# Kernel optimization log

Measured on AMD Instinct MI355X. Metric: run time of the kernel, lower is better.

## Reference

```python
import jax, jax.numpy as jnp
import numpy as np

B, T, D, H, O, L = 64, 1024, 64, 512, 1, 1


def setup_inputs() -> dict:
    key = jax.random.key(0)
    k = jax.random.split(key, 6)
    s = 1.0 / np.sqrt(H)  # PyTorch GRU init scale U(-1/sqrt(H), 1/sqrt(H))
    x = jax.random.normal(k[0], (B, T, D), dtype=jnp.float32)
    h = jnp.zeros((L, B, H), dtype=jnp.float32)
    w_ih = jax.random.uniform(k[1], (3 * H, D), jnp.float32, -s, s)
    w_hh = jax.random.uniform(k[2], (3 * H, H), jnp.float32, -s, s)
    fc_w = jax.random.uniform(k[3], (O, H), jnp.float32, -s, s)
    fc_b = jax.random.uniform(k[4], (O,), jnp.float32, -s, s)
    return {"x": x, "h": h, "w_ih": w_ih, "w_hh": w_hh, "fc_w": fc_w, "fc_b": fc_b}


def _gru_layer(x, h0, w_ih, w_hh):
    # x: [B,T,D], h0: [B,H]. bias=False GRU, PyTorch gate order r,z,n.
    Hd = w_hh.shape[1]
    gi_all = jnp.einsum('btd,gd->tbg', x, w_ih)  # [T,B,3H] input projections, one big GEMM

    def step(h, gi):
        gh = h @ w_hh.T  # [B,3H]
        r = jax.nn.sigmoid(gi[:, :Hd] + gh[:, :Hd])
        z = jax.nn.sigmoid(gi[:, Hd:2 * Hd] + gh[:, Hd:2 * Hd])
        n = jnp.tanh(gi[:, 2 * Hd:] + r * gh[:, 2 * Hd:])
        h_new = (1.0 - z) * n + z * h
        return h_new, h_new

    h_last, hs = jax.lax.scan(step, h0, gi_all)  # hs: [T,B,H]
    return jnp.swapaxes(hs, 0, 1), h_last  # [B,T,H], [B,H]


def reference(x, h, w_ih, w_hh, fc_w, fc_b):
    out_seq, h_last = _gru_layer(x, h[0], w_ih, w_hh)
    out = jax.nn.relu(out_seq) @ fc_w.T + fc_b  # [B,T,O]
    return out, h_last[None]  # h: [n_layers=1, B, H]
```

## Files before the change

kernel.cpp:

```cpp
#include <hip/hip_runtime.h>

typedef short bf16x8 __attribute__((ext_vector_type(8)));
typedef float f32x4  __attribute__((ext_vector_type(4)));
typedef unsigned int u32;
typedef unsigned long long u64;

constexpr int BB = 64;
constexpr int TT = 1024;
constexpr int DD = 64;
constexpr int HH = 512;
constexpr int NGRP = 8;
constexpr int WPG  = 16;
constexpr int MB   = 8;
constexpr int UPW  = 32;
constexpr int BLOCK = 384;

constexpr size_t SLAB_U64  = (size_t)MB * 256;
constexpr size_t BOARD_U64 = 2 * NGRP * SLAB_U64;
constexpr size_t BOARD_B   = BOARD_U64 * 8;

__device__ __forceinline__ short f2bf(float f) {
    unsigned u = __builtin_bit_cast(unsigned, f);
    u = (u + 0x7FFFu + ((u >> 16) & 1u)) >> 16;
    return (short)u;
}
__device__ __forceinline__ float bf2f(short s) {
    unsigned u = ((unsigned)(unsigned short)s) << 16;
    return __builtin_bit_cast(float, u);
}

constexpr int LROW = 80;
constexpr int LKK  = 656;

__global__ __launch_bounds__(BLOCK, 2)
void gru_persistent(const float* __restrict__ x,
                    const float* __restrict__ h0,
                    const float* __restrict__ w_ih,
                    const float* __restrict__ w_hh,
                    const float* __restrict__ fc_w,
                    const float* __restrict__ fc_b,
                    float* __restrict__ out,
                    u64* __restrict__ board)
{
    const int wg   = blockIdx.x;
    const int gb   = wg & 7;
    const int wid  = wg >> 3;
    const int tid  = threadIdx.x;
    const int wave = tid >> 6;
    const int lane = tid & 63;
    const int l15  = lane & 15;
    const int lhi  = lane >> 4;
    const int u0   = wid * UPW;

    const int cloc = wave * 16 + l15;
    const int grow = (cloc >> 5) * HH + u0 + (cloc & 31);

    __shared__ char  lds_board[16 * LKK];
    __shared__ float lds_gi[8][100];
    __shared__ float lds_gh[8][100];
    __shared__ float fcw_lds[HH];

    bf16x8 whh_hi[16], whh_lo[16];
#pragma unroll
    for (int kk = 0; kk < 16; ++kk) {
        const float* src = w_hh + (size_t)grow * HH + kk * 32 + lhi * 8;
        bf16x8 hi, lo;
#pragma unroll
        for (int i = 0; i < 8; ++i) {
            float w = src[i];
            short h16 = f2bf(w);
            hi[i] = h16; lo[i] = f2bf(w - bf2f(h16));
        }
        whh_hi[kk] = hi; whh_lo[kk] = lo;
    }
    bf16x8 wih_hi[2], wih_lo[2];
#pragma unroll
    for (int kk = 0; kk < 2; ++kk) {
        const float* src = w_ih + (size_t)grow * DD + kk * 32 + lhi * 8;
        bf16x8 hi, lo;
#pragma unroll
        for (int i = 0; i < 8; ++i) {
            float w = src[i];
            short h16 = f2bf(w);
            hi[i] = h16; lo[i] = f2bf(w - bf2f(h16));
        }
        wih_hi[kk] = hi; wih_lo[kk] = lo;
    }

    for (int i = tid; i < HH; i += BLOCK) fcw_lds[i] = fc_w[i];
    const float fcb = fc_b[0];

    float hreg0 = 0.f, hreg1 = 0.f;
    if (tid < 128) {
        int row = tid >> 4, lp = tid & 15;
        hreg0 = h0[(size_t)(gb * MB + row) * HH + (u0 + 2 * lp)];
        hreg1 = h0[(size_t)(gb * MB + row) * HH + (u0 + 2 * lp + 1)];
        u32 wa = (1u << 16) | (u32)(unsigned short)f2bf(hreg0);
        u32 wb = (1u << 16) | (u32)(unsigned short)f2bf(hreg1);
        u64* bw = board + (size_t)(0 * NGRP + gb) * SLAB_U64 + row * 256 + (wid * 16 + lp);
        __hip_atomic_store(bw, (u64)wa | ((u64)wb << 32),
                           __ATOMIC_RELAXED, __HIP_MEMORY_SCOPE_AGENT);
    }
    __syncthreads();

    const float* xrow = x + ((size_t)(gb * MB + (l15 & 7)) * TT) * DD + lhi * 8;

    for (int t = 0; t <= TT; ++t) {
        const int rbuf = t & 1, wbuf = rbuf ^ 1;

        u64 v[8];
        const u64* sp = board + (size_t)(rbuf * NGRP + gb) * SLAB_U64 + tid;
        if (tid < 256) {
#pragma unroll
            for (int i = 0; i < 8; ++i)
                v[i] = __hip_atomic_load(sp + (size_t)i * 256,
                                         __ATOMIC_RELAXED, __HIP_MEMORY_SCOPE_AGENT);
        }

        f32x4 acc_gi = {0.f, 0.f, 0.f, 0.f};
        if (t < TT) {
            f32x4 gi_hi = {0.f,0.f,0.f,0.f}, gi_lo = {0.f,0.f,0.f,0.f};
#pragma unroll
            for (int kk = 0; kk < 2; ++kk) {
                const float* xs = xrow + (size_t)t * DD + kk * 32;
                const float4 v0 = *(const float4*)(xs);
                const float4 v1 = *(const float4*)(xs + 4);
                bf16x8 a;
                a[0] = f2bf(v0.x); a[1] = f2bf(v0.y); a[2] = f2bf(v0.z); a[3] = f2bf(v0.w);
                a[4] = f2bf(v1.x); a[5] = f2bf(v1.y); a[6] = f2bf(v1.z); a[7] = f2bf(v1.w);
                gi_hi = __builtin_amdgcn_mfma_f32_16x16x32_bf16(a, wih_hi[kk], gi_hi, 0, 0, 0);
                gi_lo = __builtin_amdgcn_mfma_f32_16x16x32_bf16(a, wih_lo[kk], gi_lo, 0, 0, 0);
            }
            acc_gi = gi_hi + gi_lo;
        }

        if (tid < 256) {
            const u32 expTag = (u32)(t + 1) << 16;
            while (true) {
                u32 bad = 0;
#pragma unroll
                for (int i = 0; i < 8; ++i) {
                    u32 lo = (u32)v[i], hi = (u32)(v[i] >> 32);
                    bad |= ((lo ^ expTag) | (hi ^ expTag)) & 0xFFFF0000u;
                }
                if (!__any(bad != 0)) break;
#pragma unroll
                for (int i = 0; i < 8; ++i)
                    v[i] = __hip_atomic_load(sp + (size_t)i * 256,
                                             __ATOMIC_RELAXED, __HIP_MEMORY_SCOPE_AGENT);
            }
            char* lb = lds_board + (tid >> 4) * LKK + (tid & 15) * 4;
#pragma unroll
            for (int i = 0; i < 8; ++i) {
                u32 d = __builtin_amdgcn_perm((u32)(v[i] >> 32), (u32)v[i], 0x05040100u);
                *(u32*)(lb + i * LROW) = d;
            }
        }
        __syncthreads();

        if (wave == 0 && wid < MB && t >= 1) {
            const char* lb = lds_board + (lane >> 2) * LKK + wid * LROW + (lane & 3) * 16;
            bf16x8 hv = *(const bf16x8*)lb;
            float s = 0.f;
#pragma unroll
            for (int i = 0; i < 8; ++i)
                s += fmaxf(bf2f(hv[i]), 0.f) * fcw_lds[lane * 8 + i];
#pragma unroll
            for (int off = 1; off < 64; off <<= 1) s += __shfl_xor(s, off, 64);
            if (lane == 0)
                out[(size_t)(gb * MB + wid) * TT + (t - 1)] = s + fcb;
        }
        if (t == TT) break;

        f32x4 gh_hi = {0.f,0.f,0.f,0.f}, gh_lo = {0.f,0.f,0.f,0.f};
        {
            const char* la = lds_board + (l15 & 7) * LROW + lhi * 16;
#pragma unroll
            for (int kk = 0; kk < 16; ++kk) {
                bf16x8 a = *(const bf16x8*)(la + kk * LKK);
                gh_hi = __builtin_amdgcn_mfma_f32_16x16x32_bf16(a, whh_hi[kk], gh_hi, 0, 0, 0);
                gh_lo = __builtin_amdgcn_mfma_f32_16x16x32_bf16(a, whh_lo[kk], gh_lo, 0, 0, 0);
            }
        }
        f32x4 acc_gh = gh_hi + gh_lo;

        if (lhi < 2) {
#pragma unroll
            for (int j = 0; j < 4; ++j) {
                int row = lhi * 4 + j;
                lds_gi[row][cloc] = acc_gi[j];
                lds_gh[row][cloc] = acc_gh[j];
            }
        }
        __syncthreads();

        if (tid < 128) {
            const u32 tagNew = (u32)(t + 2) << 16;
            int row = tid >> 4, lp = tid & 15;
            int uu0 = 2 * lp, uu1 = uu0 + 1;
            float hn01[2];
            float hp[2] = {hreg0, hreg1};
#pragma unroll
            for (int q = 0; q < 2; ++q) {
                int uu = uu0 + q;
                float gr  = lds_gi[row][uu]      + lds_gh[row][uu];
                float gz  = lds_gi[row][32 + uu] + lds_gh[row][32 + uu];
                float gin = lds_gi[row][64 + uu];
                float ghn = lds_gh[row][64 + uu];
                float r = 1.f / (1.f + __expf(-gr));
                float z = 1.f / (1.f + __expf(-gz));
                float vv = gin + r * ghn;
                vv = fminf(15.f, fmaxf(-15.f, vv));
                float e2 = __expf(-2.f * vv);
                float n = (1.f - e2) / (1.f + e2);
                hn01[q] = (1.f - z) * n + z * hp[q];
            }
            hreg0 = hn01[0]; hreg1 = hn01[1];
            u32 wa = tagNew | (u32)(unsigned short)f2bf(hn01[0]);
            u32 wb = tagNew | (u32)(unsigned short)f2bf(hn01[1]);
            u64* bw = board + (size_t)(wbuf * NGRP + gb) * SLAB_U64
                    + row * 256 + (wid * 16 + lp);
            __hip_atomic_store(bw, (u64)wa | ((u64)wb << 32),
                               __ATOMIC_RELAXED, __HIP_MEMORY_SCOPE_AGENT);
            if (t == TT - 1) {
                out[(size_t)BB * TT + (size_t)(gb * MB + row) * HH + (u0 + uu0)] = hn01[0];
                out[(size_t)BB * TT + (size_t)(gb * MB + row) * HH + (u0 + uu1)] = hn01[1];
            }
        }
    }
}

extern "C" void kernel_launch(void* const* d_in, const int* in_sizes, int n_in,
                              void* d_out, int out_size, void* d_ws, size_t ws_size,
                              hipStream_t stream)
{
    const float* x    = (const float*)d_in[0];
    const float* h0   = (const float*)d_in[1];
    const float* w_ih = (const float*)d_in[2];
    const float* w_hh = (const float*)d_in[3];
    const float* fc_w = (const float*)d_in[4];
    const float* fc_b = (const float*)d_in[5];
    float* out = (float*)d_out;
    u64* board = (u64*)d_ws;

    hipMemsetAsync(d_ws, 0, BOARD_B, stream);

    void* args[] = { (void*)&x, (void*)&h0, (void*)&w_ih, (void*)&w_hh,
                     (void*)&fc_w, (void*)&fc_b, (void*)&out, (void*)&board };
    hipError_t err = hipLaunchCooperativeKernel((void*)gru_persistent,
                                                dim3(NGRP * WPG), dim3(BLOCK),
                                                args, 0, stream);
    if (err != hipSuccess) {
        (void)hipGetLastError();
        gru_persistent<<<dim3(NGRP * WPG), dim3(BLOCK), 0, stream>>>(
            x, h0, w_ih, w_hh, fc_w, fc_b, out, board);
    }
}
```

Measured before the change: 2.855 ms.

## Split each batch group into two interleaved sub-batches to overlap recurrence latency

Each workgroup now processes its 8 batch rows as two independent sub-batches of 4, alternating between them within each timestep. While one sub-batch's hidden state is being computed and published to the global board, the other sub-batch's board slab is prefetched and waited on, which is meant to hide cross-workgroup synchronisation latency. The board gains a sub-batch dimension and per-element stores become 32-bit. In exchange there are twice as many barriers and MFMA passes per step, each with half the useful rows, and the MFMA row utilisation drops.

Result: slower. 3.903 ms (+36.7%).

```diff
diff --git a/kernel.cpp b/kernel.cpp
--- a/kernel.cpp
+++ b/kernel.cpp
@@ -11,13 +11,18 @@
 constexpr int HH = 512;
 constexpr int NGRP = 8;
 constexpr int WPG  = 16;
-constexpr int MB   = 8;
+constexpr int NSB  = 2;
+constexpr int MB   = 4;
 constexpr int UPW  = 32;
 constexpr int BLOCK = 384;
 
 constexpr size_t SLAB_U64  = (size_t)MB * 256;
-constexpr size_t BOARD_U64 = 2 * NGRP * SLAB_U64;
+constexpr size_t BOARD_U64 = 2 * NSB * NGRP * SLAB_U64;
 constexpr size_t BOARD_B   = BOARD_U64 * 8;
+
+__device__ __forceinline__ size_t slab(int buf, int s, int g) {
+    return ((size_t)(buf * NSB + s) * NGRP + g) * SLAB_U64;
+}
 
 __device__ __forceinline__ short f2bf(float f) {
     unsigned u = __builtin_bit_cast(unsigned, f);
@@ -30,7 +35,7 @@
 }
 
 constexpr int LROW = 80;
-constexpr int LKK  = 656;
+constexpr int LKK  = 336;
 
 __global__ __launch_bounds__(BLOCK, 2)
 void gru_persistent(const float* __restrict__ x,
@@ -56,8 +61,8 @@
     const int grow = (cloc >> 5) * HH + u0 + (cloc & 31);
 
     __shared__ char  lds_board[16 * LKK];
-    __shared__ float lds_gi[8][100];
-    __shared__ float lds_gh[8][100];
+    __shared__ float lds_gi[4][100];
+    __shared__ float lds_gh[4][100];
     __shared__ float fcw_lds[HH];
 
     bf16x8 whh_hi[16], whh_lo[16];
@@ -90,119 +95,135 @@
     for (int i = tid; i < HH; i += BLOCK) fcw_lds[i] = fc_w[i];
     const float fcb = fc_b[0];
 
-    float hreg0 = 0.f, hreg1 = 0.f;
+    float hreg[NSB] = {0.f, 0.f};
     if (tid < 128) {
-        int row = tid >> 4, lp = tid & 15;
-        hreg0 = h0[(size_t)(gb * MB + row) * HH + (u0 + 2 * lp)];
-        hreg1 = h0[(size_t)(gb * MB + row) * HH + (u0 + 2 * lp + 1)];
-        u32 wa = (1u << 16) | (u32)(unsigned short)f2bf(hreg0);
-        u32 wb = (1u << 16) | (u32)(unsigned short)f2bf(hreg1);
-        u64* bw = board + (size_t)(0 * NGRP + gb) * SLAB_U64 + row * 256 + (wid * 16 + lp);
-        __hip_atomic_store(bw, (u64)wa | ((u64)wb << 32),
-                           __ATOMIC_RELAXED, __HIP_MEMORY_SCOPE_AGENT);
+        int row = tid >> 5, uu = tid & 31;
+#pragma unroll
+        for (int s = 0; s < NSB; ++s) {
+            float hv = h0[(size_t)(gb * 8 + s * MB + row) * HH + u0 + uu];
+            hreg[s] = hv;
+            u32 w = (1u << 16) | (u32)(unsigned short)f2bf(hv);
+            u32* bw = (u32*)(board + slab(0, s, gb)) + row * 512 + wid * 32 + uu;
+            __hip_atomic_store(bw, w, __ATOMIC_RELAXED, __HIP_MEMORY_SCOPE_AGENT);
+        }
     }
     __syncthreads();
 
-    const float* xrow = x + ((size_t)(gb * MB + (l15 & 7)) * TT) * DD + lhi * 8;
+    const float* xrow[NSB];
+#pragma unroll
+    for (int s = 0; s < NSB; ++s)
+        xrow[s] = x + ((size_t)(gb * 8 + s * MB + (l15 & 3)) * TT) * DD + lhi * 8;
+
+    u64 v[4];
+    const u64* sp = board + slab(0, 0, gb) + tid;
+    if (tid < 256) {
+#pragma unroll
+        for (int i = 0; i < 4; ++i)
+            v[i] = __hip_atomic_load(sp + (size_t)i * 256,
+                                     __ATOMIC_RELAXED, __HIP_MEMORY_SCOPE_AGENT);
+    }
 
     for (int t = 0; t <= TT; ++t) {
-        const int rbuf = t & 1, wbuf = rbuf ^ 1;
-
-        u64 v[8];
-        const u64* sp = board + (size_t)(rbuf * NGRP + gb) * SLAB_U64 + tid;
-        if (tid < 256) {
-#pragma unroll
-            for (int i = 0; i < 8; ++i)
-                v[i] = __hip_atomic_load(sp + (size_t)i * 256,
-                                         __ATOMIC_RELAXED, __HIP_MEMORY_SCOPE_AGENT);
-        }
-
-        f32x4 acc_gi = {0.f, 0.f, 0.f, 0.f};
-        if (t < TT) {
-            f32x4 gi_hi = {0.f,0.f,0.f,0.f}, gi_lo = {0.f,0.f,0.f,0.f};
-#pragma unroll
-            for (int kk = 0; kk < 2; ++kk) {
-                const float* xs = xrow + (size_t)t * DD + kk * 32;
-                const float4 v0 = *(const float4*)(xs);
-                const float4 v1 = *(const float4*)(xs + 4);
-                bf16x8 a;
-                a[0] = f2bf(v0.x); a[1] = f2bf(v0.y); a[2] = f2bf(v0.z); a[3] = f2bf(v0.w);
-                a[4] = f2bf(v1.x); a[5] = f2bf(v1.y); a[6] = f2bf(v1.z); a[7] = f2bf(v1.w);
-                gi_hi = __builtin_amdgcn_mfma_f32_16x16x32_bf16(a, wih_hi[kk], gi_hi, 0, 0, 0);
-                gi_lo = __builtin_amdgcn_mfma_f32_16x16x32_bf16(a, wih_lo[kk], gi_lo, 0, 0, 0);
-            }
-            acc_gi = gi_hi + gi_lo;
-        }
-
-        if (tid < 256) {
-            const u32 expTag = (u32)(t + 1) << 16;
-            while (true) {
-                u32 bad = 0;
-#pragma unroll
-                for (int i = 0; i < 8; ++i) {
-                    u32 lo = (u32)v[i], hi = (u32)(v[i] >> 32);
-                    bad |= ((lo ^ expTag) | (hi ^ expTag)) & 0xFFFF0000u;
-                }
-                if (!__any(bad != 0)) break;
-#pragma unroll
-                for (int i = 0; i < 8; ++i)
-                    v[i] = __hip_atomic_load(sp + (size_t)i * 256,
-                                             __ATOMIC_RELAXED, __HIP_MEMORY_SCOPE_AGENT);
-            }
-            char* lb = lds_board + (tid >> 4) * LKK + (tid & 15) * 4;
-#pragma unroll
-            for (int i = 0; i < 8; ++i) {
-                u32 d = __builtin_amdgcn_perm((u32)(v[i] >> 32), (u32)v[i], 0x05040100u);
-                *(u32*)(lb + i * LROW) = d;
-            }
-        }
-        __syncthreads();
-
-        if (wave == 0 && wid < MB && t >= 1) {
-            const char* lb = lds_board + (lane >> 2) * LKK + wid * LROW + (lane & 3) * 16;
-            bf16x8 hv = *(const bf16x8*)lb;
-            float s = 0.f;
-#pragma unroll
-            for (int i = 0; i < 8; ++i)
-                s += fmaxf(bf2f(hv[i]), 0.f) * fcw_lds[lane * 8 + i];
-#pragma unroll
-            for (int off = 1; off < 64; off <<= 1) s += __shfl_xor(s, off, 64);
-            if (lane == 0)
-                out[(size_t)(gb * MB + wid) * TT + (t - 1)] = s + fcb;
-        }
-        if (t == TT) break;
-
-        f32x4 gh_hi = {0.f,0.f,0.f,0.f}, gh_lo = {0.f,0.f,0.f,0.f};
-        {
-            const char* la = lds_board + (l15 & 7) * LROW + lhi * 16;
-#pragma unroll
-            for (int kk = 0; kk < 16; ++kk) {
-                bf16x8 a = *(const bf16x8*)(la + kk * LKK);
-                gh_hi = __builtin_amdgcn_mfma_f32_16x16x32_bf16(a, whh_hi[kk], gh_hi, 0, 0, 0);
-                gh_lo = __builtin_amdgcn_mfma_f32_16x16x32_bf16(a, whh_lo[kk], gh_lo, 0, 0, 0);
-            }
-        }
-        f32x4 acc_gh = gh_hi + gh_lo;
-
-        if (lhi < 2) {
-#pragma unroll
-            for (int j = 0; j < 4; ++j) {
-                int row = lhi * 4 + j;
-                lds_gi[row][cloc] = acc_gi[j];
-                lds_gh[row][cloc] = acc_gh[j];
-            }
-        }
-        __syncthreads();
-
-        if (tid < 128) {
-            const u32 tagNew = (u32)(t + 2) << 16;
-            int row = tid >> 4, lp = tid & 15;
-            int uu0 = 2 * lp, uu1 = uu0 + 1;
-            float hn01[2];
-            float hp[2] = {hreg0, hreg1};
-#pragma unroll
-            for (int q = 0; q < 2; ++q) {
-                int uu = uu0 + q;
+#pragma unroll
+        for (int s = 0; s < NSB; ++s) {
+            const int wbuf = (t & 1) ^ 1;
+
+            f32x4 acc_gi = {0.f, 0.f, 0.f, 0.f};
+            if (t < TT) {
+                f32x4 gih = {0.f,0.f,0.f,0.f}, gil = {0.f,0.f,0.f,0.f};
+#pragma unroll
+                for (int kk = 0; kk < 2; ++kk) {
+                    const float* xs = xrow[s] + (size_t)t * DD + kk * 32;
+                    const float4 v0 = *(const float4*)(xs);
+                    const float4 v1 = *(const float4*)(xs + 4);
+                    bf16x8 a;
+                    a[0] = f2bf(v0.x); a[1] = f2bf(v0.y); a[2] = f2bf(v0.z); a[3] = f2bf(v0.w);
+                    a[4] = f2bf(v1.x); a[5] = f2bf(v1.y); a[6] = f2bf(v1.z); a[7] = f2bf(v1.w);
+                    gih = __builtin_amdgcn_mfma_f32_16x16x32_bf16(a, wih_hi[kk], gih, 0, 0, 0);
+                    gil = __builtin_amdgcn_mfma_f32_16x16x32_bf16(a, wih_lo[kk], gil, 0, 0, 0);
+                }
+                acc_gi = gih + gil;
+            }
+
+            if (tid < 256) {
+                const u32 expTag = (u32)(t + 1) << 16;
+                while (true) {
+                    u32 bad = 0;
+#pragma unroll
+                    for (int i = 0; i < 4; ++i) {
+                        u32 lo = (u32)v[i], hi = (u32)(v[i] >> 32);
+                        bad |= ((lo ^ expTag) | (hi ^ expTag)) & 0xFFFF0000u;
+                    }
+                    if (!__any(bad != 0)) break;
+#pragma unroll
+                    for (int i = 0; i < 4; ++i)
+                        v[i] = __hip_atomic_load(sp + (size_t)i * 256,
+                                                 __ATOMIC_RELAXED, __HIP_MEMORY_SCOPE_AGENT);
+                }
+                char* lb = lds_board + (tid >> 4) * LKK + (tid & 15) * 4;
+#pragma unroll
+                for (int i = 0; i < 4; ++i) {
+                    u32 d = __builtin_amdgcn_perm((u32)(v[i] >> 32), (u32)v[i], 0x05040100u);
+                    *(u32*)(lb + i * LROW) = d;
+                }
+            }
+            __syncthreads();
+
+            {
+                const int ns = s ^ 1;
+                const int nt = (s == 1) ? t + 1 : t;
+                if (nt <= TT) {
+                    sp = board + slab(nt & 1, ns, gb) + tid;
+                    if (tid < 256) {
+#pragma unroll
+                        for (int i = 0; i < 4; ++i)
+                            v[i] = __hip_atomic_load(sp + (size_t)i * 256,
+                                                     __ATOMIC_RELAXED, __HIP_MEMORY_SCOPE_AGENT);
+                    }
+                }
+            }
+
+            {
+                const int rs = wid - s * MB;
+                if (wave == 0 && (unsigned)rs < (unsigned)MB && t >= 1) {
+                    const char* lb = lds_board + (lane >> 2) * LKK + rs * LROW + (lane & 3) * 16;
+                    bf16x8 hv = *(const bf16x8*)lb;
+                    float ss = 0.f;
+#pragma unroll
+                    for (int i = 0; i < 8; ++i)
+                        ss += fmaxf(bf2f(hv[i]), 0.f) * fcw_lds[lane * 8 + i];
+#pragma unroll
+                    for (int off = 1; off < 64; off <<= 1) ss += __shfl_xor(ss, off, 64);
+                    if (lane == 0)
+                        out[(size_t)(gb * 8 + s * MB + rs) * TT + (t - 1)] = ss + fcb;
+                }
+            }
+            if (t == TT) continue;
+
+            f32x4 ghh = {0.f,0.f,0.f,0.f}, ghl = {0.f,0.f,0.f,0.f};
+            {
+                const char* la = lds_board + (l15 & 3) * LROW + lhi * 16;
+#pragma unroll
+                for (int kk = 0; kk < 16; ++kk) {
+                    bf16x8 a = *(const bf16x8*)(la + kk * LKK);
+                    ghh = __builtin_amdgcn_mfma_f32_16x16x32_bf16(a, whh_hi[kk], ghh, 0, 0, 0);
+                    ghl = __builtin_amdgcn_mfma_f32_16x16x32_bf16(a, whh_lo[kk], ghl, 0, 0, 0);
+                }
+            }
+            f32x4 acc_gh = ghh + ghl;
+
+            if (lhi == 0) {
+#pragma unroll
+                for (int j = 0; j < 4; ++j) {
+                    lds_gi[j][cloc] = acc_gi[j];
+                    lds_gh[j][cloc] = acc_gh[j];
+                }
+            }
+            __syncthreads();
+
+            if (tid < 128) {
+                const u32 tagNew = (u32)(t + 2) << 16;
+                int row = tid >> 5, uu = tid & 31;
                 float gr  = lds_gi[row][uu]      + lds_gh[row][uu];
                 float gz  = lds_gi[row][32 + uu] + lds_gh[row][32 + uu];
                 float gin = lds_gi[row][64 + uu];
@@ -213,18 +234,13 @@
                 vv = fminf(15.f, fmaxf(-15.f, vv));
                 float e2 = __expf(-2.f * vv);
                 float n = (1.f - e2) / (1.f + e2);
-                hn01[q] = (1.f - z) * n + z * hp[q];
-            }
-            hreg0 = hn01[0]; hreg1 = hn01[1];
-            u32 wa = tagNew | (u32)(unsigned short)f2bf(hn01[0]);
-            u32 wb = tagNew | (u32)(unsigned short)f2bf(hn01[1]);
-            u64* bw = board + (size_t)(wbuf * NGRP + gb) * SLAB_U64
-                    + row * 256 + (wid * 16 + lp);
-            __hip_atomic_store(bw, (u64)wa | ((u64)wb << 32),
-                               __ATOMIC_RELAXED, __HIP_MEMORY_SCOPE_AGENT);
-            if (t == TT - 1) {
-                out[(size_t)BB * TT + (size_t)(gb * MB + row) * HH + (u0 + uu0)] = hn01[0];
-                out[(size_t)BB * TT + (size_t)(gb * MB + row) * HH + (u0 + uu1)] = hn01[1];
+                float hn = (1.f - z) * n + z * hreg[s];
+                hreg[s] = hn;
+                u32 w = tagNew | (u32)(unsigned short)f2bf(hn);
+                u32* bw = (u32*)(board + slab(wbuf, s, gb)) + row * 512 + wid * 32 + uu;
+                __hip_atomic_store(bw, w, __ATOMIC_RELAXED, __HIP_MEMORY_SCOPE_AGENT);
+                if (t == TT - 1)
+                    out[(size_t)BB * TT + (size_t)(gb * 8 + s * MB + row) * HH + u0 + uu] = hn;
             }
         }
     }
```
